# Kernel optimization log

Hardware: AMD Instinct MI355X
Metric: run time of the kernel (lower is better)

The kernel has to match this reference:

```python
import jax, jax.numpy as jnp
import numpy as np

N, E, F, H = 100000, 1600000, 128, 128


def setup_inputs() -> dict:
    key = jax.random.key(0)
    ks = jax.random.split(key, 32)
    def w(i, shape):
        fan_in = shape[0]
        return jax.random.normal(ks[i], shape, dtype=jnp.float32) / np.sqrt(fan_in)
    inp = {
        'x': jax.random.normal(ks[0], (N, F), dtype=jnp.float32),
        't': jax.random.randint(ks[1], (N,), 0, 2, dtype=jnp.int32),
        'z': jax.random.normal(ks[2], (N, H), dtype=jnp.float32),
        'edge_index': jax.random.randint(ks[3], (2, E), 0, N, dtype=jnp.int32),
        # GCNConv weights (PyG: out = scatter(norm * (xW)) + b)
        'W_o': w(4, (F, H)), 'b_o': jnp.zeros((H,), jnp.float32),
        'W_t': w(5, (F, H)), 'b_t': jnp.zeros((H,), jnp.float32),
        # masked attention: Linear(2H, 1)
        'a_w': w(6, (2 * H, 1)), 'a_b': jnp.zeros((1,), jnp.float32),
        # encoder_final: Linear(2H, H)
        'W_enc': w(7, (2 * H, H)), 'b_enc': jnp.zeros((H,), jnp.float32),
        # predictor heads (3 linears each)
        'p1_W1': w(8, (H, H)), 'p1_b1': jnp.zeros((H,), jnp.float32),
        'p1_W2': w(9, (H, H)), 'p1_b2': jnp.zeros((H,), jnp.float32),
        'p1_W3': w(10, (H, 1)), 'p1_b3': jnp.zeros((1,), jnp.float32),
        'p0_W1': w(11, (H, H)), 'p0_b1': jnp.zeros((H,), jnp.float32),
        'p0_W2': w(12, (H, H)), 'p0_b2': jnp.zeros((H,), jnp.float32),
        'p0_W3': w(13, (H, 1)), 'p0_b3': jnp.zeros((1,), jnp.float32),
        # discriminator head
        'd_W1': w(14, (H, H)), 'd_b1': jnp.zeros((H,), jnp.float32),
        'd_W2': w(15, (H, H)), 'd_b2': jnp.zeros((H,), jnp.float32),
        'd_W3': w(16, (H, 1)), 'd_b3': jnp.zeros((1,), jnp.float32),
    }
    return inp


def _mlp3(x, W1, b1, W2, b2, W3, b3):
    h = jax.nn.leaky_relu(x @ W1 + b1, 0.2)
    h = jax.nn.leaky_relu(h @ W2 + b2, 0.2)
    return h @ W3 + b3


def _gcn(x, W, b, src, dst, norm, n):
    xw = x @ W                                   # [N,H]
    agg = jax.ops.segment_sum(xw[src] * norm[:, None], dst, num_segments=n)
    return agg + b


def reference(x, t, z, edge_index, W_o, b_o, W_t, b_t, a_w, a_b, W_enc, b_enc,
              p1_W1, p1_b1, p1_W2, p1_b2, p1_W3, p1_b3,
              p0_W1, p0_b1, p0_W2, p0_b2, p0_W3, p0_b3,
              d_W1, d_b1, d_W2, d_b2, d_W3, d_b3):
    n = x.shape[0]
    src, dst = edge_index[0], edge_index[1]
    # --- GCN with self-loops and symmetric normalization ---
    loop = jnp.arange(n, dtype=src.dtype)
    src2 = jnp.concatenate([src, loop])
    dst2 = jnp.concatenate([dst, loop])
    deg = jax.ops.segment_sum(jnp.ones_like(dst2, jnp.float32), dst2, num_segments=n)
    dinv = jax.lax.rsqrt(deg)                    # deg >= 1 (self loops)
    norm = dinv[src2] * dinv[dst2]               # [E+N]
    r_o = jax.nn.relu(_gcn(x, W_o, b_o, src2, dst2, norm, n))
    r_t = jax.nn.relu(_gcn(x, W_t, b_t, src2, dst2, norm, n))
    cat = jnp.concatenate([r_o, r_t], axis=-1)   # [N,2H]
    # --- masked attention over edges: only treated sources attend ---
    e = (cat @ a_w + a_b)[:, 0]                  # [N]
    logits = jax.nn.leaky_relu(e[src] + e[dst], 0.2)   # [E]
    mask = (t[src] > 0).astype(jnp.float32)
    m = jax.ops.segment_max(logits, dst, num_segments=n)
    m = jnp.where(jnp.isfinite(m), m, 0.0)
    w = jnp.exp(logits - m[dst]) * mask
    denom = jax.ops.segment_sum(w, dst, num_segments=n) + 1e-16
    alpha = w / denom[dst]                       # [E]
    h = jax.ops.segment_sum(r_t[src] * alpha[:, None], dst, num_segments=n)  # [N,H]
    # --- heads ---
    z_enc = jnp.concatenate([r_o, h], axis=-1) @ W_enc + b_enc   # [N,H]
    pred_1 = _mlp3(z_enc, p1_W1, p1_b1, p1_W2, p1_b2, p1_W3, p1_b3)[:, 0]
    pred_0 = _mlp3(z_enc, p0_W1, p0_b1, p0_W2, p0_b2, p0_W3, p0_b3)[:, 0]
    pred = jnp.where(t > 0, pred_1, pred_0)[:, None]             # [N,1]
    pred_t = jax.nn.sigmoid(_mlp3(r_t, d_W1, d_b1, d_W2, d_b2, d_W3, d_b3))  # [N,1]
    return pred_t, pred, z_enc
```

## Files before the change

kernel.cpp:

```cpp
#include <hip/hip_runtime.h>
#include <hip/hip_bf16.h>
#include <math.h>


using bf16x8 = __attribute__((ext_vector_type(8))) short;
using s16x8  = __attribute__((ext_vector_type(8))) short;
using f32x4  = __attribute__((ext_vector_type(4))) float;

static __device__ __forceinline__ float lrelu02(float x) { return x > 0.f ? x : 0.2f * x; }

static __device__ __forceinline__ unsigned short f2bf(float f) {
    unsigned u = __float_as_uint(f);
    unsigned r = u + 0x7FFF + ((u >> 16) & 1);
    return (unsigned short)(r >> 16);
}
static __device__ __forceinline__ float bf2f(unsigned short h) {
    return __uint_as_float(((unsigned)h) << 16);
}
static __device__ __forceinline__ float bflo(unsigned u) { return __uint_as_float(u << 16); }
static __device__ __forceinline__ float bfhi(unsigned u) { return __uint_as_float(u & 0xFFFF0000u); }


__global__ __launch_bounds__(256) void k_bhist(const int* __restrict__ src,
                                               const int* __restrict__ dst,
                                               const int* __restrict__ t,
                                               int* __restrict__ bhist,
                                               int* __restrict__ bhist_m,
                                               int e, int shift) {
    __shared__ int h[256], hm[256];
    h[threadIdx.x] = 0; hm[threadIdx.x] = 0;
    __syncthreads();
    int i = blockIdx.x * blockDim.x + threadIdx.x;
    int stride = gridDim.x * blockDim.x;
    for (; i < e; i += stride) {
        int b = dst[i] >> shift;
        atomicAdd(&h[b], 1);
        if (t[src[i]] > 0) atomicAdd(&hm[b], 1);
    }
    __syncthreads();
    if (h[threadIdx.x]) atomicAdd(&bhist[threadIdx.x], h[threadIdx.x]);
    if (hm[threadIdx.x]) atomicAdd(&bhist_m[threadIdx.x], hm[threadIdx.x]);
}

__global__ __launch_bounds__(256) void k_scan2(const int* __restrict__ bhist,
                                               const int* __restrict__ bhist_m,
                                               int* __restrict__ bbase,
                                               int* __restrict__ bbase_m,
                                               int* __restrict__ bcur, int nb) {
    __shared__ int s[256];
    int t = threadIdx.x;
    int v = (t < nb) ? bhist[t] : 0;
    s[t] = v;
    __syncthreads();
    for (int off = 1; off < 256; off <<= 1) {
        int u = (t >= off) ? s[t - off] : 0;
        __syncthreads();
        s[t] += u;
        __syncthreads();
    }
    if (t < nb) { bbase[t] = s[t] - v; bcur[t] = s[t] - v; }
    if (t == nb - 1) bbase[nb] = s[t];
    __syncthreads();
    int v2 = (t < nb) ? bhist_m[t] : 0;
    s[t] = v2;
    __syncthreads();
    for (int off = 1; off < 256; off <<= 1) {
        int u = (t >= off) ? s[t - off] : 0;
        __syncthreads();
        s[t] += u;
        __syncthreads();
    }
    if (t < nb) bbase_m[t] = s[t] - v2;
    if (t == nb - 1) bbase_m[nb] = s[t];
}

__global__ __launch_bounds__(256) void k_fillB(const int* __restrict__ src,
                                               const int* __restrict__ dst,
                                               const int* __restrict__ t,
                                               int* __restrict__ bcur,
                                               int* __restrict__ ebuf,
                                               int e, int shift) {
    __shared__ int h[256];
    const int EPT = 16;
    int blk_base = blockIdx.x * 256 * EPT;
    h[threadIdx.x] = 0;
    __syncthreads();
    int pk[EPT], bk[EPT];
#pragma unroll
    for (int j = 0; j < EPT; ++j) {
        int i = blk_base + threadIdx.x + j * 256;
        if (i < e) {
            int s = src[i], d = dst[i];
            int b = d >> shift;
            bk[j] = b;
            int tb = (t[s] > 0) ? 1 : 0;
            pk[j] = s | ((d - (b << shift)) << 20) | (tb << 29);
            atomicAdd(&h[b], 1);
        } else bk[j] = -1;
    }
    __syncthreads();
    int cnt = h[threadIdx.x];
    int base = 0;
    if (cnt > 0) base = atomicAdd(&bcur[threadIdx.x], cnt);
    __syncthreads();
    h[threadIdx.x] = base;
    __syncthreads();
#pragma unroll
    for (int j = 0; j < EPT; ++j) {
        if (bk[j] >= 0) {
            int pos = atomicAdd(&h[bk[j]], 1);
            ebuf[pos] = pk[j];
        }
    }
}

__global__ __launch_bounds__(256) void k_sortC(const int* __restrict__ ebuf,
                                               const int* __restrict__ bbase,
                                               const int* __restrict__ bbase_m,
                                               int* __restrict__ indptr,
                                               int* __restrict__ indptr_m,
                                               float* __restrict__ dinv,
                                               int* __restrict__ out_all,
                                               int* __restrict__ out_m,
                                               int n, int shift, int NB) {
    __shared__ int cnt[512], cnt_m[512];
    __shared__ int cur[512], cur_m[512];
    __shared__ int tmp[256];
    int tid = threadIdx.x;
    int b = blockIdx.x;
    int lo = bbase[b], hi = bbase[b + 1];
    int lom = bbase_m[b];
    int dbase = b << shift;
    for (int j = tid; j < 512; j += 256) { cnt[j] = 0; cnt_m[j] = 0; }
    __syncthreads();
    for (int i = lo + tid; i < hi; i += 256) {
        int pk = ebuf[i];
        int dlo = (pk >> 20) & 511;
        atomicAdd(&cnt[dlo], 1);
        if (pk >> 29) atomicAdd(&cnt_m[dlo], 1);
    }
    __syncthreads();
    int c0 = cnt[2 * tid], c1 = cnt[2 * tid + 1];
    int ps = c0 + c1;
    tmp[tid] = ps;
    __syncthreads();
    for (int off = 1; off < 256; off <<= 1) {
        int u = (tid >= off) ? tmp[tid - off] : 0;
        __syncthreads();
        tmp[tid] += u;
        __syncthreads();
    }
    int pre = tmp[tid] - ps;
    cur[2 * tid] = pre;
    cur[2 * tid + 1] = pre + c0;
    __syncthreads();
    int m0 = cnt_m[2 * tid], m1 = cnt_m[2 * tid + 1];
    int psm = m0 + m1;
    tmp[tid] = psm;
    __syncthreads();
    for (int off = 1; off < 256; off <<= 1) {
        int u = (tid >= off) ? tmp[tid - off] : 0;
        __syncthreads();
        tmp[tid] += u;
        __syncthreads();
    }
    int prem = tmp[tid] - psm;
    cur_m[2 * tid] = prem;
    cur_m[2 * tid + 1] = prem + m0;
    __syncthreads();
    int nd = n - dbase; if (nd > 512) nd = 512;
    for (int j = tid; j < nd; j += 256) {
        indptr[dbase + j] = lo + cur[j];
        indptr_m[dbase + j] = lom + cur_m[j];
        dinv[dbase + j] = rsqrtf((float)cnt[j] + 1.0f);
    }
    if (b == 0 && tid == 0) {
        indptr[n] = bbase[NB];
        indptr_m[n] = bbase_m[NB];
    }
    __syncthreads();
    for (int i = lo + tid; i < hi; i += 256) {
        int pk = ebuf[i];
        int s = pk & 0xFFFFF;
        int dlo = (pk >> 20) & 511;
        int pos = lo + atomicAdd(&cur[dlo], 1);
        out_all[pos] = s;
        if (pk >> 29) {
            int pm = lom + atomicAdd(&cur_m[dlo], 1);
            out_m[pm] = s;
        }
    }
}


__global__ void k_cvt_pre(const float* __restrict__ x, const float* __restrict__ dinv,
                          unsigned short* __restrict__ xp, int total4) {
    int i = blockIdx.x * blockDim.x + threadIdx.x;
    int stride = gridDim.x * blockDim.x;
    for (; i < total4; i += stride) {
        float dv = dinv[i >> 5];
        float4 v = ((const float4*)x)[i];
        ushort4 o;
        o.x = f2bf(v.x * dv); o.y = f2bf(v.y * dv);
        o.z = f2bf(v.z * dv); o.w = f2bf(v.w * dv);
        ((ushort4*)xp)[i] = o;
    }
}

__global__ void k_wprep(const float* __restrict__ Wo, const float* __restrict__ Wti,
                        const float* __restrict__ Wenc,
                        const float* __restrict__ p1W1, const float* __restrict__ p1W2,
                        const float* __restrict__ p0W1, const float* __restrict__ p0W2,
                        const float* __restrict__ dW1, const float* __restrict__ dW2,
                        unsigned short* __restrict__ Wcat_t,
                        unsigned short* __restrict__ Wenc_t,
                        unsigned short* __restrict__ o1, unsigned short* __restrict__ o2,
                        unsigned short* __restrict__ o3, unsigned short* __restrict__ o4,
                        unsigned short* __restrict__ o5, unsigned short* __restrict__ o6) {
    int idx = blockIdx.x * 256 + threadIdx.x;
    if (idx < 32768) {
        int j = idx >> 7, k = idx & 127;
        float v = (j < 128) ? Wo[(k << 7) + j] : Wti[(k << 7) + j - 128];
        Wcat_t[idx] = f2bf(v);
    } else if (idx < 65536) {
        int i = idx - 32768;
        Wenc_t[(size_t)(i & 127) * 256 + (i >> 7)] = f2bf(Wenc[i]);
    } else {
        int i2 = idx - 65536;
        int h = i2 >> 14;
        int i = i2 & 16383;
        const float* W; unsigned short* O;
        switch (h) {
            case 0: W = p1W1; O = o1; break;
            case 1: W = p1W2; O = o2; break;
            case 2: W = p0W1; O = o3; break;
            case 3: W = p0W2; O = o4; break;
            case 4: W = dW1;  O = o5; break;
            default: W = dW2; O = o6; break;
        }
        O[(i & 127) * 128 + (i >> 7)] = f2bf(W[i]);
    }
}

__global__ __launch_bounds__(256) void k_aggx(const unsigned short* __restrict__ xp,
                                              const int* __restrict__ indptr,
                                              const int* __restrict__ srcs,
                                              const float* __restrict__ dinv,
                                              unsigned short* __restrict__ aggx, int n) {
    int wv = threadIdx.x >> 6, lane = threadIdx.x & 63;
    int v = blockIdx.x * 4 + wv;
    if (v >= n) return;
    const unsigned* xp2 = (const unsigned*)xp;
    int beg = indptr[v], end = indptr[v + 1];
    unsigned sv = xp2[(size_t)v * 64 + lane];
    float a0 = bflo(sv), a1 = bfhi(sv);
    int i = beg;
    for (; i + 8 <= end; i += 8) {
        int s0 = srcs[i], s1 = srcs[i + 1], s2 = srcs[i + 2], s3 = srcs[i + 3];
        int s4 = srcs[i + 4], s5 = srcs[i + 5], s6 = srcs[i + 6], s7 = srcs[i + 7];
        unsigned u0 = xp2[(size_t)s0 * 64 + lane];
        unsigned u1 = xp2[(size_t)s1 * 64 + lane];
        unsigned u2 = xp2[(size_t)s2 * 64 + lane];
        unsigned u3 = xp2[(size_t)s3 * 64 + lane];
        unsigned u4 = xp2[(size_t)s4 * 64 + lane];
        unsigned u5 = xp2[(size_t)s5 * 64 + lane];
        unsigned u6 = xp2[(size_t)s6 * 64 + lane];
        unsigned u7 = xp2[(size_t)s7 * 64 + lane];
        a0 += bflo(u0) + bflo(u1) + bflo(u2) + bflo(u3)
            + bflo(u4) + bflo(u5) + bflo(u6) + bflo(u7);
        a1 += bfhi(u0) + bfhi(u1) + bfhi(u2) + bfhi(u3)
            + bfhi(u4) + bfhi(u5) + bfhi(u6) + bfhi(u7);
    }
    for (; i + 4 <= end; i += 4) {
        int s0 = srcs[i], s1 = srcs[i + 1], s2 = srcs[i + 2], s3 = srcs[i + 3];
        unsigned u0 = xp2[(size_t)s0 * 64 + lane];
        unsigned u1 = xp2[(size_t)s1 * 64 + lane];
        unsigned u2 = xp2[(size_t)s2 * 64 + lane];
        unsigned u3 = xp2[(size_t)s3 * 64 + lane];
        a0 += bflo(u0) + bflo(u1) + bflo(u2) + bflo(u3);
        a1 += bfhi(u0) + bfhi(u1) + bfhi(u2) + bfhi(u3);
    }
    for (; i < end; ++i) {
        unsigned u = xp2[(size_t)srcs[i] * 64 + lane];
        a0 += bflo(u); a1 += bfhi(u);
    }
    float dv = dinv[v];
    a0 *= dv; a1 *= dv;
    unsigned o = (unsigned)f2bf(a0) | ((unsigned)f2bf(a1) << 16);
    ((unsigned*)aggx)[(size_t)v * 64 + lane] = o;
}

__global__ __launch_bounds__(256) void k_gcn(const unsigned short* __restrict__ aggx,
                                             const unsigned short* __restrict__ Wcat,
                                             const float* __restrict__ b_o,
                                             const float* __restrict__ b_t,
                                             const float* __restrict__ a_w,
                                             const float* __restrict__ a_b,
                                             unsigned short* __restrict__ cat2,
                                             unsigned short* __restrict__ rt,
                                             float* __restrict__ e, int M) {
    __shared__ short ct[64][264];
    int wave = threadIdx.x >> 6, lane = threadIdx.x & 63;
    int row_base = blockIdx.x * 64 + wave * 16;
    int rA = row_base + (lane & 15);
    if (rA >= M) rA = M - 1;
    int koff = (lane >> 4) << 3;
    int colL = lane & 15;

    bf16x8 a[4];
#pragma unroll
    for (int ks = 0; ks < 4; ++ks)
        a[ks] = *(const bf16x8*)((const short*)aggx + (size_t)rA * 128 + (ks << 5) + koff);

    f32x4 acc[16];
#pragma unroll
    for (int cf = 0; cf < 16; ++cf) acc[cf] = (f32x4){0.f, 0.f, 0.f, 0.f};
#pragma unroll
    for (int ks = 0; ks < 4; ++ks)
#pragma unroll
        for (int cf = 0; cf < 16; ++cf) {
            bf16x8 b = *(const bf16x8*)((const short*)Wcat + (size_t)((cf << 4) + colL) * 128 + (ks << 5) + koff);
            acc[cf] = __builtin_amdgcn_mfma_f32_16x16x32_bf16(a[ks], b, acc[cf], 0, 0, 0);
        }

    float ep0 = 0.f, ep1 = 0.f, ep2 = 0.f, ep3 = 0.f;
    int rl0 = wave * 16 + ((lane >> 4) << 2);
#pragma unroll
    for (int cf = 0; cf < 16; ++cf) {
        int col = (cf << 4) + colL;
        float bv = (col < 128) ? b_o[col] : b_t[col - 128];
        float aw = a_w[col];
#pragma unroll
        for (int j = 0; j < 4; ++j) {
            float v = fmaxf(acc[cf][j] + bv, 0.f);
            if (j == 0) ep0 += v * aw;
            else if (j == 1) ep1 += v * aw;
            else if (j == 2) ep2 += v * aw;
            else ep3 += v * aw;
            ct[rl0 + j][col] = (short)f2bf(v);
        }
    }
#pragma unroll
    for (int mk = 1; mk < 16; mk <<= 1) {
        ep0 += __shfl_xor(ep0, mk); ep1 += __shfl_xor(ep1, mk);
        ep2 += __shfl_xor(ep2, mk); ep3 += __shfl_xor(ep3, mk);
    }
    if (colL == 0) {
        float ab = a_b[0];
        int r0 = row_base + ((lane >> 4) << 2);
        if (r0 + 0 < M) e[r0 + 0] = ep0 + ab;
        if (r0 + 1 < M) e[r0 + 1] = ep1 + ab;
        if (r0 + 2 < M) e[r0 + 2] = ep2 + ab;
        if (r0 + 3 < M) e[r0 + 3] = ep3 + ab;
    }
    __syncthreads();
    int base64 = blockIdx.x * 64;
    short* cp = (short*)cat2 + (size_t)base64 * 256;
    for (int j = threadIdx.x; j < 1024; j += 256) {
        int row = j >> 4;
        if (base64 + row < M)
            *(s16x8*)(cp + (size_t)row * 256 + ((j & 15) << 3)) =
                *(const s16x8*)&ct[row][(j & 15) << 3];
    }
    short* rp = (short*)rt + (size_t)base64 * 128;
    for (int j = threadIdx.x; j < 1024; j += 256) {
        int row = j >> 4;
        if (base64 + row < M)
            *(s16x8*)(rp + (size_t)row * 128 + ((j & 15) << 3)) =
                *(const s16x8*)&ct[row][128 + ((j & 15) << 3)];
    }
}

__global__ __launch_bounds__(256) void k_attn(const unsigned short* __restrict__ rt,
                                              const int* __restrict__ indptr_m,
                                              const int* __restrict__ srcs_m,
                                              const float* __restrict__ e,
                                              unsigned short* __restrict__ cat2, int n) {
    int wv = threadIdx.x >> 6, lane = threadIdx.x & 63;
    int v = blockIdx.x * 4 + wv;
    if (v >= n) return;
    float ev = e[v];
    int bm = indptr_m[v], em = indptr_m[v + 1];
    float m = -INFINITY;
    for (int i = bm + lane; i < em; i += 64)
        m = fmaxf(m, lrelu02(ev + e[srcs_m[i]]));
    for (int off = 32; off; off >>= 1) m = fmaxf(m, __shfl_xor(m, off));
    if (bm == em) m = 0.f;
    float h0 = 0.f, h1 = 0.f, wsum = 0.f;
    const unsigned* rt2 = (const unsigned*)rt;
    int i = bm;
    for (; i + 8 <= em; i += 8) {
        int s0 = srcs_m[i], s1 = srcs_m[i + 1], s2 = srcs_m[i + 2], s3 = srcs_m[i + 3];
        int s4 = srcs_m[i + 4], s5 = srcs_m[i + 5], s6 = srcs_m[i + 6], s7 = srcs_m[i + 7];
        float w0 = __expf(lrelu02(ev + e[s0]) - m);
        float w1 = __expf(lrelu02(ev + e[s1]) - m);
        float w2 = __expf(lrelu02(ev + e[s2]) - m);
        float w3 = __expf(lrelu02(ev + e[s3]) - m);
        float w4 = __expf(lrelu02(ev + e[s4]) - m);
        float w5 = __expf(lrelu02(ev + e[s5]) - m);
        float w6 = __expf(lrelu02(ev + e[s6]) - m);
        float w7 = __expf(lrelu02(ev + e[s7]) - m);
        unsigned u0 = rt2[(size_t)s0 * 64 + lane];
        unsigned u1 = rt2[(size_t)s1 * 64 + lane];
        unsigned u2 = rt2[(size_t)s2 * 64 + lane];
        unsigned u3 = rt2[(size_t)s3 * 64 + lane];
        unsigned u4 = rt2[(size_t)s4 * 64 + lane];
        unsigned u5 = rt2[(size_t)s5 * 64 + lane];
        unsigned u6 = rt2[(size_t)s6 * 64 + lane];
        unsigned u7 = rt2[(size_t)s7 * 64 + lane];
        wsum += w0 + w1 + w2 + w3 + w4 + w5 + w6 + w7;
        h0 += w0 * bflo(u0) + w1 * bflo(u1) + w2 * bflo(u2) + w3 * bflo(u3)
            + w4 * bflo(u4) + w5 * bflo(u5) + w6 * bflo(u6) + w7 * bflo(u7);
        h1 += w0 * bfhi(u0) + w1 * bfhi(u1) + w2 * bfhi(u2) + w3 * bfhi(u3)
            + w4 * bfhi(u4) + w5 * bfhi(u5) + w6 * bfhi(u6) + w7 * bfhi(u7);
    }
    for (; i < em; ++i) {
        int s = srcs_m[i];
        float w = __expf(lrelu02(ev + e[s]) - m);
        unsigned u = rt2[(size_t)s * 64 + lane];
        wsum += w;
        h0 += w * bflo(u);
        h1 += w * bfhi(u);
    }
    float inv = 1.f / (wsum + 1e-16f);
    unsigned o = (unsigned)f2bf(h0 * inv) | ((unsigned)f2bf(h1 * inv) << 16);
    ((unsigned*)(cat2 + (size_t)v * 256 + 128))[lane] = o;
}

__global__ __launch_bounds__(512) void k_tail(
    const unsigned short* __restrict__ cat2, const unsigned short* __restrict__ rt_bf,
    const unsigned short* __restrict__ Wenc, const float* __restrict__ b_enc,
    const unsigned short* __restrict__ W11, const float* __restrict__ b11,
    const unsigned short* __restrict__ W12, const float* __restrict__ b12,
    const float* __restrict__ W13, const float* __restrict__ b13,
    const unsigned short* __restrict__ W01, const float* __restrict__ b01,
    const unsigned short* __restrict__ W02, const float* __restrict__ b02,
    const float* __restrict__ W03, const float* __restrict__ b03,
    const unsigned short* __restrict__ Wd1, const float* __restrict__ bd1,
    const unsigned short* __restrict__ Wd2, const float* __restrict__ bd2,
    const float* __restrict__ Wd3, const float* __restrict__ bd3,
    const int* __restrict__ t, float* __restrict__ zenc,
    float* __restrict__ out, int M) {
    __shared__ __align__(16) char pool[128 * 136 * 2 + 128 * 136 * 2];
    short* Wa = (short*)pool;
    short* hb = (short*)(pool + 128 * 136 * 2);
    float* zt = (float*)pool;

    int wave = threadIdx.x >> 6, lane = threadIdx.x & 63;
    int colL = lane & 15;
    int koff = (lane >> 4) << 3;
    int base128 = blockIdx.x * 128;
    int rA = base128 + wave * 16 + colL;
    if (rA >= M) rA = M - 1;

    bf16x8 ra[4];
#pragma unroll
    for (int ks = 0; ks < 4; ++ks)
        ra[ks] = *(const bf16x8*)((const short*)rt_bf + (size_t)rA * 128 + (ks << 5) + koff);

    f32x4 acc1[8];
    {
        const short* Ap = (const short*)cat2 + (size_t)rA * 256 + koff;
        const short* Bp = (const short*)Wenc + (size_t)colL * 256 + koff;
#pragma unroll
        for (int cf = 0; cf < 8; ++cf) acc1[cf] = (f32x4){0.f, 0.f, 0.f, 0.f};
#pragma unroll
        for (int ks = 0; ks < 8; ++ks) {
            bf16x8 a = *(const bf16x8*)(Ap + (ks << 5));
#pragma unroll
            for (int cf = 0; cf < 8; ++cf) {
                bf16x8 b = *(const bf16x8*)(Bp + (size_t)(cf << 4) * 256 + (ks << 5));
                acc1[cf] = __builtin_amdgcn_mfma_f32_16x16x32_bf16(a, b, acc1[cf], 0, 0, 0);
            }
        }
    }

    bf16x8 za[4];
#pragma unroll
    for (int chunk = 0; chunk < 2; ++chunk) {
        if ((wave >> 2) == chunk) {
            int rl0 = (wave & 3) * 16 + ((lane >> 4) << 2);
#pragma unroll
            for (int cf = 0; cf < 8; ++cf) {
                int col = (cf << 4) + colL;
                float bv = b_enc[col];
#pragma unroll
                for (int j = 0; j < 4; ++j)
                    zt[(rl0 + j) * 132 + col] = acc1[cf][j] + bv;
            }
        }
        __syncthreads();
        {
            int gbase = base128 + chunk * 64;
            float* zp = zenc + (size_t)gbase * 128;
            for (int j = threadIdx.x; j < 2048; j += 512) {
                int row = j >> 5;
                if (gbase + row < M)
                    *(float4*)(zp + (size_t)j * 4) = *(const float4*)&zt[row * 132 + ((j & 31) << 2)];
            }
        }
        if ((wave >> 2) == chunk) {
            int rAl = (wave & 3) * 16 + colL;
#pragma unroll
            for (int ks = 0; ks < 4; ++ks) {
                float4 v0 = *(const float4*)&zt[rAl * 132 + (ks << 5) + koff];
                float4 v1 = *(const float4*)&zt[rAl * 132 + (ks << 5) + koff + 4];
                za[ks][0] = (short)f2bf(v0.x); za[ks][1] = (short)f2bf(v0.y);
                za[ks][2] = (short)f2bf(v0.z); za[ks][3] = (short)f2bf(v0.w);
                za[ks][4] = (short)f2bf(v1.x); za[ks][5] = (short)f2bf(v1.y);
                za[ks][6] = (short)f2bf(v1.z); za[ks][7] = (short)f2bf(v1.w);
            }
        }
        __syncthreads();
    }

    float sp1[4], sp0[4], sdd[4];

    auto stage = [&](const unsigned short* W) {
        for (int i = threadIdx.x; i < 2048; i += 512) {
            int r = i >> 4, c = (i & 15) << 3;
            bf16x8 v = *(const bf16x8*)((const short*)W + (r << 7) + c);
            *(bf16x8*)(Wa + r * 136 + c) = v;
        }
    };

    auto run_head = [&](const bf16x8* A0,
                        const unsigned short* W1, const float* b1,
                        const unsigned short* W2, const float* b2,
                        const float* W3, const float* b3, float* sout) {
        __syncthreads();
        stage(W1);
        __syncthreads();
        f32x4 acc[8];
#pragma unroll
        for (int cf = 0; cf < 8; ++cf) acc[cf] = (f32x4){0.f, 0.f, 0.f, 0.f};
#pragma unroll
        for (int ks = 0; ks < 4; ++ks)
#pragma unroll
            for (int cf = 0; cf < 8; ++cf) {
                bf16x8 b = *(const bf16x8*)(Wa + ((cf << 4) + colL) * 136 + (ks << 5) + koff);
                acc[cf] = __builtin_amdgcn_mfma_f32_16x16x32_bf16(A0[ks], b, acc[cf], 0, 0, 0);
            }
        short* hw = hb + wave * 2176;
#pragma unroll
        for (int cf = 0; cf < 8; ++cf) {
            int col = (cf << 4) + colL;
            float bv = b1[col];
#pragma unroll
            for (int j = 0; j < 4; ++j)
                hw[(((lane >> 4) << 2) + j) * 136 + col] = (short)f2bf(lrelu02(acc[cf][j] + bv));
        }
        __syncthreads();
        stage(W2);
        __syncthreads();
        bf16x8 h1f[4];
#pragma unroll
        for (int ks = 0; ks < 4; ++ks)
            h1f[ks] = *(const bf16x8*)(hw + colL * 136 + (ks << 5) + koff);
#pragma unroll
        for (int cf = 0; cf < 8; ++cf) acc[cf] = (f32x4){0.f, 0.f, 0.f, 0.f};
#pragma unroll
        for (int ks = 0; ks < 4; ++ks)
#pragma unroll
            for (int cf = 0; cf < 8; ++cf) {
                bf16x8 b = *(const bf16x8*)(Wa + ((cf << 4) + colL) * 136 + (ks << 5) + koff);
                acc[cf] = __builtin_amdgcn_mfma_f32_16x16x32_bf16(h1f[ks], b, acc[cf], 0, 0, 0);
            }
        float s0 = 0.f, s1 = 0.f, s2 = 0.f, s3 = 0.f;
#pragma unroll
        for (int cf = 0; cf < 8; ++cf) {
            int col = (cf << 4) + colL;
            float w3 = W3[col], bv = b2[col];
            s0 += lrelu02(acc[cf][0] + bv) * w3;
            s1 += lrelu02(acc[cf][1] + bv) * w3;
            s2 += lrelu02(acc[cf][2] + bv) * w3;
            s3 += lrelu02(acc[cf][3] + bv) * w3;
        }
#pragma unroll
        for (int mk = 1; mk < 16; mk <<= 1) {
            s0 += __shfl_xor(s0, mk); s1 += __shfl_xor(s1, mk);
            s2 += __shfl_xor(s2, mk); s3 += __shfl_xor(s3, mk);
        }
        float bb = b3[0];
        sout[0] = s0 + bb; sout[1] = s1 + bb; sout[2] = s2 + bb; sout[3] = s3 + bb;
    };

    run_head(za, W11, b11, W12, b12, W13, b13, sp1);
    run_head(za, W01, b01, W02, b02, W03, b03, sp0);
    run_head(ra, Wd1, bd1, Wd2, bd2, Wd3, bd3, sdd);

    if (colL == 0) {
#pragma unroll
        for (int j = 0; j < 4; ++j) {
            int row = base128 + wave * 16 + ((lane >> 4) << 2) + j;
            if (row < M) {
                out[row] = 1.f / (1.f + __expf(-sdd[j]));
                out[M + row] = (t[row] > 0) ? sp1[j] : sp0[j];
            }
        }
    }
}


extern "C" void kernel_launch(void* const* d_in, const int* in_sizes, int n_in,
                              void* d_out, int out_size, void* d_ws, size_t ws_size,
                              hipStream_t stream) {
    const float* x     = (const float*)d_in[0];
    const int*   t     = (const int*)d_in[1];
    const int*   ei    = (const int*)d_in[3];
    const float* W_o   = (const float*)d_in[4];
    const float* b_o   = (const float*)d_in[5];
    const float* W_t   = (const float*)d_in[6];
    const float* b_t   = (const float*)d_in[7];
    const float* a_w   = (const float*)d_in[8];
    const float* a_b   = (const float*)d_in[9];
    const float* W_enc = (const float*)d_in[10];
    const float* b_enc = (const float*)d_in[11];
    const float* p1_W1 = (const float*)d_in[12]; const float* p1_b1 = (const float*)d_in[13];
    const float* p1_W2 = (const float*)d_in[14]; const float* p1_b2 = (const float*)d_in[15];
    const float* p1_W3 = (const float*)d_in[16]; const float* p1_b3 = (const float*)d_in[17];
    const float* p0_W1 = (const float*)d_in[18]; const float* p0_b1 = (const float*)d_in[19];
    const float* p0_W2 = (const float*)d_in[20]; const float* p0_b2 = (const float*)d_in[21];
    const float* p0_W3 = (const float*)d_in[22]; const float* p0_b3 = (const float*)d_in[23];
    const float* d_W1  = (const float*)d_in[24]; const float* d_b1  = (const float*)d_in[25];
    const float* d_W2  = (const float*)d_in[26]; const float* d_b2  = (const float*)d_in[27];
    const float* d_W3  = (const float*)d_in[28]; const float* d_b3  = (const float*)d_in[29];

    const int n = in_sizes[1];
    const int E = in_sizes[3] / 2;
    const int* src = ei;
    const int* dst = ei + E;

    float* out  = (float*)d_out;
    float* zenc = out + 2 * (size_t)n;

    const int shift = 9;
    const int NB = (n + (1 << shift) - 1) >> shift;

    char* base = (char*)d_ws;
    size_t o = 0;
    auto alloc = [&](size_t bytes) { char* p = base + o; o += (bytes + 255) & ~(size_t)255; return p; };
    unsigned short* xp_bf   = (unsigned short*)alloc((size_t)n * 128 * 2);
    unsigned short* aggx_bf = (unsigned short*)alloc((size_t)n * 128 * 2);
    unsigned short* cat2_bf = (unsigned short*)alloc((size_t)n * 256 * 2);
    unsigned short* rt_bf   = (unsigned short*)alloc((size_t)n * 128 * 2);
    float* dinv = (float*)alloc((size_t)n * 4);
    float* evec = (float*)alloc((size_t)n * 4);
    unsigned short* Wcat_t = (unsigned short*)alloc(256 * 128 * 2);
    unsigned short* Wenc_t = (unsigned short*)alloc(128 * 256 * 2);
    unsigned short* Wp1a_t = (unsigned short*)alloc(128 * 128 * 2);
    unsigned short* Wp1b_t = (unsigned short*)alloc(128 * 128 * 2);
    unsigned short* Wp0a_t = (unsigned short*)alloc(128 * 128 * 2);
    unsigned short* Wp0b_t = (unsigned short*)alloc(128 * 128 * 2);
    unsigned short* Wda_t  = (unsigned short*)alloc(128 * 128 * 2);
    unsigned short* Wdb_t  = (unsigned short*)alloc(128 * 128 * 2);
    int* indptr     = (int*)alloc(((size_t)n + 1) * 4);
    int* indptr_m   = (int*)alloc(((size_t)n + 1) * 4);
    int* bhist      = (int*)alloc(514 * 4);
    int* bhist_m    = bhist + 257;
    int* bbase      = (int*)alloc(257 * 4);
    int* bbase_m    = (int*)alloc(257 * 4);
    int* bcur       = (int*)alloc(257 * 4);
    int* src_sorted = (int*)alloc((size_t)E * 4);
    int* src_mask   = (int*)alloc((size_t)E * 4);
    int* ebuf       = (int*)alloc((size_t)E * 4);

    const int mt  = (n + 63) / 64;
    const int mt2 = (n + 127) / 128;

    hipMemsetAsync(bhist, 0, 514 * 4, stream);
    k_bhist<<<1024, 256, 0, stream>>>(src, dst, t, bhist, bhist_m, E, shift);
    k_scan2<<<1, 256, 0, stream>>>(bhist, bhist_m, bbase, bbase_m, bcur, NB);
    k_fillB<<<(E + 4095) / 4096, 256, 0, stream>>>(src, dst, t, bcur, ebuf, E, shift);
    k_sortC<<<NB, 256, 0, stream>>>(ebuf, bbase, bbase_m, indptr, indptr_m, dinv,
                                    src_sorted, src_mask, n, shift, NB);

    k_wprep<<<640, 256, 0, stream>>>(W_o, W_t, W_enc, p1_W1, p1_W2, p0_W1, p0_W2,
                                     d_W1, d_W2, Wcat_t, Wenc_t,
                                     Wp1a_t, Wp1b_t, Wp0a_t, Wp0b_t, Wda_t, Wdb_t);
    k_cvt_pre<<<2048, 256, 0, stream>>>(x, dinv, xp_bf, n * 32);

    k_aggx<<<(n + 3) / 4, 256, 0, stream>>>(xp_bf, indptr, src_sorted, dinv, aggx_bf, n);

    k_gcn<<<mt, 256, 0, stream>>>(aggx_bf, Wcat_t, b_o, b_t, a_w, a_b,
                                  cat2_bf, rt_bf, evec, n);

    k_attn<<<(n + 3) / 4, 256, 0, stream>>>(rt_bf, indptr_m, src_mask, evec, cat2_bf, n);

    k_tail<<<mt2, 512, 0, stream>>>(cat2_bf, rt_bf, Wenc_t, b_enc,
                                    Wp1a_t, p1_b1, Wp1b_t, p1_b2, p1_W3, p1_b3,
                                    Wp0a_t, p0_b1, Wp0b_t, p0_b2, p0_W3, p0_b3,
                                    Wda_t, d_b1, Wdb_t, d_b2, d_W3, d_b3,
                                    t, zenc, out, n);
}
```

Baseline: 430.6 us.

## Drop histogram pass by binning edges into fixed-capacity per-bucket slots

```diff
diff --git a/kernel.cpp b/kernel.cpp
--- a/kernel.cpp
+++ b/kernel.cpp
@@ -2,6 +2,8 @@
 #include <hip/hip_bf16.h>
 #include <math.h>
 
+
+#define BCAP 12288
 
 using bf16x8 = __attribute__((ext_vector_type(8))) short;
 using s16x8  = __attribute__((ext_vector_type(8))) short;
@@ -21,69 +23,17 @@
 static __device__ __forceinline__ float bfhi(unsigned u) { return __uint_as_float(u & 0xFFFF0000u); }
 
 
-__global__ __launch_bounds__(256) void k_bhist(const int* __restrict__ src,
-                                               const int* __restrict__ dst,
-                                               const int* __restrict__ t,
-                                               int* __restrict__ bhist,
-                                               int* __restrict__ bhist_m,
-                                               int e, int shift) {
-    __shared__ int h[256], hm[256];
-    h[threadIdx.x] = 0; hm[threadIdx.x] = 0;
-    __syncthreads();
-    int i = blockIdx.x * blockDim.x + threadIdx.x;
-    int stride = gridDim.x * blockDim.x;
-    for (; i < e; i += stride) {
-        int b = dst[i] >> shift;
-        atomicAdd(&h[b], 1);
-        if (t[src[i]] > 0) atomicAdd(&hm[b], 1);
-    }
-    __syncthreads();
-    if (h[threadIdx.x]) atomicAdd(&bhist[threadIdx.x], h[threadIdx.x]);
-    if (hm[threadIdx.x]) atomicAdd(&bhist_m[threadIdx.x], hm[threadIdx.x]);
-}
-
-__global__ __launch_bounds__(256) void k_scan2(const int* __restrict__ bhist,
-                                               const int* __restrict__ bhist_m,
-                                               int* __restrict__ bbase,
-                                               int* __restrict__ bbase_m,
-                                               int* __restrict__ bcur, int nb) {
-    __shared__ int s[256];
-    int t = threadIdx.x;
-    int v = (t < nb) ? bhist[t] : 0;
-    s[t] = v;
-    __syncthreads();
-    for (int off = 1; off < 256; off <<= 1) {
-        int u = (t >= off) ? s[t - off] : 0;
-        __syncthreads();
-        s[t] += u;
-        __syncthreads();
-    }
-    if (t < nb) { bbase[t] = s[t] - v; bcur[t] = s[t] - v; }
-    if (t == nb - 1) bbase[nb] = s[t];
-    __syncthreads();
-    int v2 = (t < nb) ? bhist_m[t] : 0;
-    s[t] = v2;
-    __syncthreads();
-    for (int off = 1; off < 256; off <<= 1) {
-        int u = (t >= off) ? s[t - off] : 0;
-        __syncthreads();
-        s[t] += u;
-        __syncthreads();
-    }
-    if (t < nb) bbase_m[t] = s[t] - v2;
-    if (t == nb - 1) bbase_m[nb] = s[t];
-}
-
 __global__ __launch_bounds__(256) void k_fillB(const int* __restrict__ src,
                                                const int* __restrict__ dst,
                                                const int* __restrict__ t,
-                                               int* __restrict__ bcur,
+                                               int* __restrict__ pcur,
+                                               int* __restrict__ pcnt_m,
                                                int* __restrict__ ebuf,
                                                int e, int shift) {
-    __shared__ int h[256];
+    __shared__ int h[256], hm[256];
     const int EPT = 16;
     int blk_base = blockIdx.x * 256 * EPT;
-    h[threadIdx.x] = 0;
+    h[threadIdx.x] = 0; hm[threadIdx.x] = 0;
     __syncthreads();
     int pk[EPT], bk[EPT];
 #pragma unroll
@@ -96,12 +46,15 @@
             int tb = (t[s] > 0) ? 1 : 0;
             pk[j] = s | ((d - (b << shift)) << 20) | (tb << 29);
             atomicAdd(&h[b], 1);
+            if (tb) atomicAdd(&hm[b], 1);
         } else bk[j] = -1;
     }
     __syncthreads();
     int cnt = h[threadIdx.x];
     int base = 0;
-    if (cnt > 0) base = atomicAdd(&bcur[threadIdx.x], cnt);
+    if (cnt > 0) base = atomicAdd(&pcur[threadIdx.x], cnt);
+    int cm = hm[threadIdx.x];
+    if (cm > 0) atomicAdd(&pcnt_m[threadIdx.x], cm);
     __syncthreads();
     h[threadIdx.x] = base;
     __syncthreads();
@@ -109,9 +62,41 @@
     for (int j = 0; j < EPT; ++j) {
         if (bk[j] >= 0) {
             int pos = atomicAdd(&h[bk[j]], 1);
-            ebuf[pos] = pk[j];
-        }
-    }
+            if (pos < BCAP)
+                ebuf[(size_t)bk[j] * BCAP + pos] = pk[j];
+        }
+    }
+}
+
+__global__ __launch_bounds__(256) void k_scan2(const int* __restrict__ bhist,
+                                               const int* __restrict__ bhist_m,
+                                               int* __restrict__ bbase,
+                                               int* __restrict__ bbase_m, int nb) {
+    __shared__ int s[256];
+    int t = threadIdx.x;
+    int v = (t < nb) ? bhist[t] : 0;
+    s[t] = v;
+    __syncthreads();
+    for (int off = 1; off < 256; off <<= 1) {
+        int u = (t >= off) ? s[t - off] : 0;
+        __syncthreads();
+        s[t] += u;
+        __syncthreads();
+    }
+    if (t < nb) bbase[t] = s[t] - v;
+    if (t == nb - 1) bbase[nb] = s[t];
+    __syncthreads();
+    int v2 = (t < nb) ? bhist_m[t] : 0;
+    s[t] = v2;
+    __syncthreads();
+    for (int off = 1; off < 256; off <<= 1) {
+        int u = (t >= off) ? s[t - off] : 0;
+        __syncthreads();
+        s[t] += u;
+        __syncthreads();
+    }
+    if (t < nb) bbase_m[t] = s[t] - v2;
+    if (t == nb - 1) bbase_m[nb] = s[t];
 }
 
 __global__ __launch_bounds__(256) void k_sortC(const int* __restrict__ ebuf,
@@ -128,13 +113,15 @@
     __shared__ int tmp[256];
     int tid = threadIdx.x;
     int b = blockIdx.x;
-    int lo = bbase[b], hi = bbase[b + 1];
+    int lo = bbase[b];
+    int cnt_tot = bbase[b + 1] - lo;
     int lom = bbase_m[b];
+    const int* eb = ebuf + (size_t)b * BCAP;
     int dbase = b << shift;
     for (int j = tid; j < 512; j += 256) { cnt[j] = 0; cnt_m[j] = 0; }
     __syncthreads();
-    for (int i = lo + tid; i < hi; i += 256) {
-        int pk = ebuf[i];
+    for (int i = tid; i < cnt_tot; i += 256) {
+        int pk = eb[i];
         int dlo = (pk >> 20) & 511;
         atomicAdd(&cnt[dlo], 1);
         if (pk >> 29) atomicAdd(&cnt_m[dlo], 1);
@@ -179,8 +166,8 @@
         indptr_m[n] = bbase_m[NB];
     }
     __syncthreads();
-    for (int i = lo + tid; i < hi; i += 256) {
-        int pk = ebuf[i];
+    for (int i = tid; i < cnt_tot; i += 256) {
+        int pk = eb[i];
         int s = pk & 0xFFFFF;
         int dlo = (pk >> 20) & 511;
         int pos = lo + atomicAdd(&cur[dlo], 1);
@@ -656,22 +643,20 @@
     unsigned short* Wdb_t  = (unsigned short*)alloc(128 * 128 * 2);
     int* indptr     = (int*)alloc(((size_t)n + 1) * 4);
     int* indptr_m   = (int*)alloc(((size_t)n + 1) * 4);
-    int* bhist      = (int*)alloc(514 * 4);
-    int* bhist_m    = bhist + 257;
+    int* pcur       = (int*)alloc(514 * 4);
+    int* pcnt_m     = pcur + 257;
     int* bbase      = (int*)alloc(257 * 4);
     int* bbase_m    = (int*)alloc(257 * 4);
-    int* bcur       = (int*)alloc(257 * 4);
     int* src_sorted = (int*)alloc((size_t)E * 4);
     int* src_mask   = (int*)alloc((size_t)E * 4);
-    int* ebuf       = (int*)alloc((size_t)E * 4);
+    int* ebuf       = (int*)alloc((size_t)256 * BCAP * 4);
 
     const int mt  = (n + 63) / 64;
     const int mt2 = (n + 127) / 128;
 
-    hipMemsetAsync(bhist, 0, 514 * 4, stream);
-    k_bhist<<<1024, 256, 0, stream>>>(src, dst, t, bhist, bhist_m, E, shift);
-    k_scan2<<<1, 256, 0, stream>>>(bhist, bhist_m, bbase, bbase_m, bcur, NB);
-    k_fillB<<<(E + 4095) / 4096, 256, 0, stream>>>(src, dst, t, bcur, ebuf, E, shift);
+    hipMemsetAsync(pcur, 0, 514 * 4, stream);
+    k_fillB<<<(E + 4095) / 4096, 256, 0, stream>>>(src, dst, t, pcur, pcnt_m, ebuf, E, shift);
+    k_scan2<<<1, 256, 0, stream>>>(pcur, pcnt_m, bbase, bbase_m, NB);
     k_sortC<<<NB, 256, 0, stream>>>(ebuf, bbase, bbase_m, indptr, indptr_m, dinv,
                                     src_sorted, src_mask, n, shift, NB);
 
```

New measurement: 399.5 us. -7.2%, faster.
